# Kernel tuning notes

Hardware: AMD Instinct MI355X
Metric: run time of the kernel (lower is better)

Reference implementation:

```python
import jax, jax.numpy as jnp
import numpy as np

H = 256                      # latent_channels = LSTM hidden
OC = [32, 64, 64, 128]       # out_channels per mesh level
V = [5023, 1256, 314, 79, 20]  # vertex counts per level (fine -> coarse)
L = 9                        # spiral length
T = 64                       # audio frames (batch for decoder)


def setup_inputs() -> dict:
    key = jax.random.key(0)
    ks = iter(jax.random.split(key, 80))
    f32 = jnp.float32

    def nrm(shape, fan_in):
        return jax.random.normal(next(ks), shape, f32) * (1.0 / np.sqrt(fan_in))

    inp = {}
    inp['audio'] = jax.random.normal(next(ks), (T, 768), f32)
    inp['actor'] = jax.random.normal(next(ks), (V[0], 3), f32)

    # 5-layer bidirectional LSTM; layer 0 input 768, layers 1-4 input 2H
    inp['lstm_Wih0'] = nrm((2, 4 * H, 768), 768)
    inp['lstm_Whh0'] = nrm((2, 4 * H, H), H)
    inp['lstm_b0'] = jnp.zeros((2, 4 * H), f32)
    inp['lstm_Wih'] = nrm((4, 2, 4 * H, 2 * H), 2 * H)
    inp['lstm_Whh'] = nrm((4, 2, 4 * H, H), H)
    inp['lstm_b'] = jnp.zeros((4, 2, 4 * H), f32)

    # decoder entry fc: 2*latent -> num_vert * oc[-1]
    inp['fc_W'] = nrm((V[4] * OC[3], 2 * H), 2 * H)
    inp['fc_b'] = jnp.zeros((V[4] * OC[3],), f32)

    # SpiralConv weights (torch Linear layout: [out, in*L])
    inp['conv3_W'] = nrm((128, 128 * L), 128 * L); inp['conv3_b'] = jnp.zeros((128,), f32)
    inp['conv2_W'] = nrm((64, 128 * L), 128 * L);  inp['conv2_b'] = jnp.zeros((64,), f32)
    inp['conv1_W'] = nrm((64, 64 * L), 64 * L);    inp['conv1_b'] = jnp.zeros((64,), f32)
    inp['conv0_W'] = nrm((32, 64 * L), 64 * L);    inp['conv0_b'] = jnp.zeros((32,), f32)
    inp['head_W'] = nrm((3, 32 * L), 32 * L);      inp['head_b'] = jnp.zeros((3,), f32)

    # spiral indices per level: [V_j, L] with values in [0, V_j)
    for j in range(4):
        inp[f'idx{j}'] = jax.random.randint(next(ks), (V[j], L), 0, V[j], jnp.int32)

    # up_transform[j] sparse [V_j, V_{j+1}], ~3 nnz per row (COO)
    for j in range(4):
        nnz = 3 * V[j]
        inp[f'rows{j}'] = jnp.repeat(jnp.arange(V[j], dtype=jnp.int32), 3)
        inp[f'cols{j}'] = jax.random.randint(next(ks), (nnz,), 0, V[j + 1], jnp.int32)
        inp[f'vals{j}'] = jax.random.uniform(next(ks), (nnz,), f32) / 3.0
    return inp


def _lstm_dir(x, Wih, Whh, b, reverse):
    # x: [T, Din]; torch gate order i, f, g, o
    def step(carry, xt):
        h, c = carry
        g = Wih @ xt + Whh @ h + b            # [4H]
        i, f, gg, o = jnp.split(g, 4)
        c = jax.nn.sigmoid(f) * c + jax.nn.sigmoid(i) * jnp.tanh(gg)
        h = jax.nn.sigmoid(o) * jnp.tanh(c)
        return (h, c), h
    init = (jnp.zeros((H,), x.dtype), jnp.zeros((H,), x.dtype))
    _, hs = jax.lax.scan(step, init, x, reverse=reverse)
    return hs  # [T, H], aligned with input order


def _bilstm(x, Wih, Whh, b):
    hf = _lstm_dir(x, Wih[0], Whh[0], b[0], False)
    hb = _lstm_dir(x, Wih[1], Whh[1], b[1], True)
    return jnp.concatenate([hf, hb], axis=-1)  # [T, 2H]


def _pool(x, rows, cols, vals, n_out):
    # sparse up-transform: out[t, r] = sum_nnz vals * x[t, cols]
    g = x[:, cols, :] * vals[None, :, None]                       # [T, nnz, C]
    return jax.ops.segment_sum(g.swapaxes(0, 1), rows, num_segments=n_out).swapaxes(0, 1)


def _spiral(x, idx, W, b):
    # gather fixed spiral neighborhoods then dense linear
    g = x[:, idx, :].reshape(x.shape[0], idx.shape[0], -1)        # [T, V, L*C]
    return g @ W.T + b


def reference(audio, actor, lstm_Wih0, lstm_Whh0, lstm_b0, lstm_Wih, lstm_Whh, lstm_b,
              fc_W, fc_b, conv3_W, conv3_b, conv2_W, conv2_b, conv1_W, conv1_b,
              conv0_W, conv0_b, head_W, head_b,
              vals3, vals2, vals1, vals0,
              idx0, idx1, idx2, idx3,
              rows3, cols3, rows2, cols2, rows1, cols1, rows0, cols0):
    # audio embedding: 5-layer bidirectional LSTM (batch = 1)
    z = _bilstm(audio, lstm_Wih0, lstm_Whh0, lstm_b0)
    for l in range(4):
        z = _bilstm(z, lstm_Wih[l], lstm_Whh[l], lstm_b[l])       # [T, 2H]

    # decode
    x = (z @ fc_W.T + fc_b).reshape(z.shape[0], V[4], OC[3])      # [T, 20, 128]
    x = jax.nn.elu(_spiral(_pool(x, rows3, cols3, vals3, V[3]), idx3, conv3_W, conv3_b))
    x = jax.nn.elu(_spiral(_pool(x, rows2, cols2, vals2, V[2]), idx2, conv2_W, conv2_b))
    x = jax.nn.elu(_spiral(_pool(x, rows1, cols1, vals1, V[1]), idx1, conv1_W, conv1_b))
    x = jax.nn.elu(_spiral(_pool(x, rows0, cols0, vals0, V[0]), idx0, conv0_W, conv0_b))
    x = _spiral(x, idx0, head_W, head_b)                          # [T, 5023, 3]
    return x + actor[None]
```

## Files before the change

kernel.cpp:

```cpp
#include <hip/hip_runtime.h>
#include <hip/hip_bf16.h>

typedef __attribute__((ext_vector_type(8))) __bf16 bf16x8;
typedef __attribute__((ext_vector_type(4))) float  f32x4;
typedef __attribute__((ext_vector_type(4))) int    i32x4;

#define SCOPE_AGENT __HIP_MEMORY_SCOPE_AGENT

static __device__ __forceinline__ f32x4 mfma16(bf16x8 a, bf16x8 b, f32x4 c) {
    return __builtin_amdgcn_mfma_f32_16x16x32_bf16(a, b, c, 0, 0, 0);
}
static __device__ __forceinline__ i32x4 mfma_i8(i32x4 a, i32x4 b, i32x4 c) {
    return __builtin_amdgcn_mfma_i32_16x16x64_i8(a, b, c, 0, 0, 0);
}
static __device__ __forceinline__ float sigm(float x)  { return 1.0f / (1.0f + __expf(-x)); }
static __device__ __forceinline__ float tanh_(float x) { return 1.0f - 2.0f / (__expf(2.0f * x) + 1.0f); }

static __device__ __forceinline__ bf16x8 cvt8(const float* __restrict__ p) {
    const float4* q = (const float4*)p;
    float4 a = q[0], b = q[1];
    bf16x8 r;
    r[0] = (__bf16)a.x; r[1] = (__bf16)a.y; r[2] = (__bf16)a.z; r[3] = (__bf16)a.w;
    r[4] = (__bf16)b.x; r[5] = (__bf16)b.y; r[6] = (__bf16)b.z; r[7] = (__bf16)b.w;
    return r;
}
static __device__ __forceinline__ void signal_add(unsigned int* p) {
    __hip_atomic_fetch_add(p, 1u, __ATOMIC_RELEASE, SCOPE_AGENT);
}
template <int SLP>
static __device__ __forceinline__ void wait_eq(unsigned int* p, unsigned int v) {
    while (__hip_atomic_load(p, __ATOMIC_RELAXED, SCOPE_AGENT) != v)
        __builtin_amdgcn_s_sleep(SLP);
    (void)__hip_atomic_load(p, __ATOMIC_ACQUIRE, SCOPE_AGENT);
}
union g4u { unsigned long long q; __bf16 h[4]; };

#define ZBUF_OFF   1024
#define GX_OFF     132096
#define CONVW_OFF  66560
#define ARENA_A    621248
#define ARENA_B    21195456
#define WHHQ_BOFF  11534336
#define SWP_BOFF   14155776

__global__ __launch_bounds__(256) void precvt_whh(
    const float* __restrict__ Whh0, const float* __restrict__ WhhL,
    signed char* __restrict__ WhhQ, float* __restrict__ swp)
{
    const int g  = blockIdx.x * 4 + (threadIdx.x >> 6);
    const int dl = g >> 10;
    const int r  = g & 1023;
    const int lane = threadIdx.x & 63;
    const float* src = (dl < 2 ? Whh0 + (size_t)dl * 262144
                               : WhhL + (size_t)(dl - 2) * 262144) + (size_t)r * 256;
    float4 v = *(const float4*)(src + lane * 4);
    float am = fmaxf(fmaxf(fabsf(v.x), fabsf(v.y)), fmaxf(fabsf(v.z), fabsf(v.w)));
    #pragma unroll
    for (int m = 1; m < 64; m <<= 1) am = fmaxf(am, __shfl_xor(am, m));
    const float inv = am > 0.f ? 127.f / am : 0.f;
    int q0 = __float2int_rn(v.x * inv), q1 = __float2int_rn(v.y * inv);
    int q2 = __float2int_rn(v.z * inv), q3 = __float2int_rn(v.w * inv);
    unsigned pk = (q0 & 255) | ((q1 & 255) << 8) | ((q2 & 255) << 16) | ((q3 & 255) << 24);
    const int gate = r >> 8, cell = r & 255;
    const int m  = cell * 4 + gate;
    const int ln = m & 15, mt = m >> 4;
    const int k  = lane * 4;
    const int kc = k >> 6, quad = (k >> 4) & 3, j = k & 15;
    size_t addr = ((((size_t)dl * 64 + mt) * 4 + kc) * 64 + (quad * 16 + ln)) * 16 + j;
    *(unsigned*)(WhhQ + addr) = pk;
    if (lane == 0) swp[(size_t)dl * 1024 + cell * 4 + gate] = am / 127.f;
}

__global__ __launch_bounds__(256) void precvt_dec(
    const float* __restrict__ fcW, const float* __restrict__ c3W,
    const float* __restrict__ c2W, const float* __restrict__ c1W,
    const float* __restrict__ c0W, const float* __restrict__ hW,
    __bf16* __restrict__ fcWb, __bf16* __restrict__ convWb)
{
    int f = (blockIdx.x * 256 + threadIdx.x) * 4;
    if (f >= 1588064) return;
    const float* src; int off; __bf16* dst; int doff;
    if (f < 1310720) { src = fcW; off = f; dst = fcWb; doff = f; }
    else {
        int g = f - 1310720; dst = convWb; doff = g;
        if (g < 147456)      { src = c3W; off = g; }
        else if (g < 221184) { src = c2W; off = g - 147456; }
        else if (g < 258048) { src = c1W; off = g - 221184; }
        else if (g < 276480) { src = c0W; off = g - 258048; }
        else                 { src = hW;  off = g - 276480; }
    }
    float4 v = *(const float4*)(src + off);
    g4u u;
    u.h[0] = (__bf16)v.x; u.h[1] = (__bf16)v.y; u.h[2] = (__bf16)v.z; u.h[3] = (__bf16)v.w;
    *(unsigned long long*)(dst + doff) = u.q;
}

__global__ __launch_bounds__(512) __attribute__((amdgpu_waves_per_eu(2, 2)))
void lstm_fused(
    const float* __restrict__ audio,
    const float* __restrict__ Wih0,
    const float* __restrict__ WihL,
    const signed char* __restrict__ WhhQ,
    const float* __restrict__ swp,
    const float* __restrict__ b0, const float* __restrict__ bL,
    unsigned short* __restrict__ Gx_g,
    unsigned int* __restrict__ flags,
    unsigned short* __restrict__ zbuf)
{
    const int bid = blockIdx.x;
    const int tid = threadIdx.x;
    const int wave = tid >> 6, lane = tid & 63, ln = lane & 15, quad = lane >> 4;

    __shared__ __align__(16) signed char    hq[2][256];
    __shared__ __align__(16) signed char    zq[16384];
    __shared__ __align__(16) unsigned short gx_l[65536];

    if (bid < 16) {
        const int dir = bid >> 3, sub = bid & 7;
        const int gmt = sub * 8 + wave;
        const int m_a = gmt * 16 + ln;
        const int r_a = (m_a & 3) * 256 + (m_a >> 2);

        {
            const float* Wih_l = Wih0 + (size_t)dir * 786432;
            const float* b_l   = b0 + (size_t)dir * 1024;
            f32x4 acc[4];
            #pragma unroll
            for (int nt = 0; nt < 4; ++nt) acc[nt] = (f32x4){0.f, 0.f, 0.f, 0.f};
            for (int kc = 0; kc < 24; ++kc) {
                const int k0 = kc * 32 + quad * 8;
                bf16x8 afr = cvt8(Wih_l + (size_t)r_a * 768 + k0);
                #pragma unroll
                for (int nt = 0; nt < 4; ++nt) {
                    const int t = nt * 16 + ln;
                    bf16x8 bfr = cvt8(audio + (size_t)t * 768 + k0);
                    acc[nt] = mfma16(afr, bfr, acc[nt]);
                }
            }
            float bv[4];
            #pragma unroll
            for (int reg = 0; reg < 4; ++reg) {
                const int m_row = gmt * 16 + quad * 4 + reg;
                bv[reg] = b_l[(m_row & 3) * 256 + (m_row >> 2)];
            }
            #pragma unroll
            for (int nt = 0; nt < 4; ++nt)
                #pragma unroll
                for (int reg = 0; reg < 4; ++reg) {
                    const int m_row = gmt * 16 + quad * 4 + reg;
                    const int t = nt * 16 + ln;
                    __bf16 v = (__bf16)(acc[nt][reg] + bv[reg]);
                    Gx_g[(size_t)dir * 65536 + t * 1024 + m_row] =
                        __builtin_bit_cast(unsigned short, v);
                }
            __syncthreads();
            if (tid == 0) { __threadfence(); signal_add(&flags[0 * 2 + dir]); }
        }

        for (int l = 1; l < 5; ++l) {
            const float* Wih_l = WihL + (size_t)((l - 1) * 2 + dir) * 524288;
            const float* b_l   = bL + (size_t)((l - 1) * 2 + dir) * 1024;
            bf16x8 afr[16];
            #pragma unroll
            for (int kc = 0; kc < 16; ++kc)
                afr[kc] = cvt8(Wih_l + (size_t)r_a * 512 + kc * 32 + quad * 8);
            if (tid == 0) wait_eq<4>(&flags[32 + (l - 1)], 2u);
            __syncthreads();
            const __bf16* zp = (const __bf16*)(zbuf + (size_t)((l - 1) & 1) * 32768);

            f32x4 acc[4];
            #pragma unroll
            for (int nt = 0; nt < 4; ++nt) acc[nt] = (f32x4){0.f, 0.f, 0.f, 0.f};
            #pragma unroll 4
            for (int kc = 0; kc < 16; ++kc) {
                const int k0 = kc * 32 + quad * 8;
                #pragma unroll
                for (int nt = 0; nt < 4; ++nt) {
                    const int t = nt * 16 + ln;
                    bf16x8 bfr = *(const bf16x8*)(zp + (size_t)t * 512 + k0);
                    acc[nt] = mfma16(afr[kc], bfr, acc[nt]);
                }
            }
            float bv[4];
            #pragma unroll
            for (int reg = 0; reg < 4; ++reg) {
                const int m_row = gmt * 16 + quad * 4 + reg;
                bv[reg] = b_l[(m_row & 3) * 256 + (m_row >> 2)];
            }
            #pragma unroll
            for (int nt = 0; nt < 4; ++nt)
                #pragma unroll
                for (int reg = 0; reg < 4; ++reg) {
                    const int m_row = gmt * 16 + quad * 4 + reg;
                    const int t = nt * 16 + ln;
                    __bf16 v = (__bf16)(acc[nt][reg] + bv[reg]);
                    Gx_g[(size_t)dir * 65536 + t * 1024 + m_row] =
                        __builtin_bit_cast(unsigned short, v);
                }
            __syncthreads();
            if (tid == 0) { __threadfence(); signal_add(&flags[l * 2 + dir]); }
        }
    } else {
        const int dir = bid - 16;
        const unsigned short* Gx_d = Gx_g + (size_t)dir * 65536;
        const bool owner = (ln < 8);
        const int cell = wave * 32 + ln * 4 + quad;
        const int gcell = owner ? cell : 0;
        const i32x4 czero = (i32x4){0, 0, 0, 0};

        for (int l = 0; l < 5; ++l) {
            const int dl = l * 2 + dir;
            i32x4 wf[8][4];
            const i32x4* wb = (const i32x4*)(WhhQ + (size_t)dl * 262144);
            #pragma unroll
            for (int i = 0; i < 8; ++i)
                #pragma unroll
                for (int kc = 0; kc < 4; ++kc)
                    wf[i][kc] = wb[(size_t)(((wave * 8 + i) * 4 + kc)) * 64 + lane];
            float sc0 = 0.f, sc1 = 0.f, sc2 = 0.f, sc3 = 0.f;
            if (owner) {
                float4 s4 = *(const float4*)(swp + (size_t)dl * 1024 + cell * 4);
                const float f = 1.f / 127.f;
                sc0 = s4.x * f; sc1 = s4.y * f; sc2 = s4.z * f; sc3 = s4.w * f;
            }
            if (tid == 0) wait_eq<1>(&flags[l * 2 + dir], 8u);
            __syncthreads();
            {
                const float4* src = (const float4*)Gx_d;
                float4* dst = (float4*)gx_l;
                #pragma unroll
                for (int i = 0; i < 16; ++i) dst[i * 512 + tid] = src[i * 512 + tid];
            }
            if (tid < 64) ((unsigned int*)hq[0])[tid] = 0;
            float cst = 0.f;
            __syncthreads();

            for (int s = 0; s < 64; ++s) {
                const int t = dir ? (63 - s) : s;
                const int cur = s & 1, nxt = cur ^ 1;
                g4u gx;
                gx.q = *(const unsigned long long*)&gx_l[t * 1024 + gcell * 4];
                i32x4 acc[8];
                {
                    i32x4 b0v = *(const i32x4*)&hq[cur][quad * 16];
                    #pragma unroll
                    for (int i = 0; i < 8; ++i) acc[i] = mfma_i8(wf[i][0], b0v, czero);
                }
                #pragma unroll
                for (int kc = 1; kc < 4; ++kc) {
                    i32x4 b = *(const i32x4*)&hq[cur][kc * 64 + quad * 16];
                    #pragma unroll
                    for (int i = 0; i < 8; ++i) acc[i] = mfma_i8(wf[i][kc], b, acc[i]);
                }
                i32x4 a = acc[0];
                #pragma unroll
                for (int j = 1; j < 8; ++j) if (ln == j) a = acc[j];
                if (owner) {
                    float gi = (float)a[0] * sc0 + (float)gx.h[0];
                    float gf = (float)a[1] * sc1 + (float)gx.h[1];
                    float gg = (float)a[2] * sc2 + (float)gx.h[2];
                    float go = (float)a[3] * sc3 + (float)gx.h[3];
                    cst = sigm(gf) * cst + sigm(gi) * tanh_(gg);
                    float h = sigm(go) * tanh_(cst);
                    int q = __float2int_rn(h * 127.f);
                    hq[nxt][cell] = (signed char)q;
                    zq[t * 256 + cell] = (signed char)q;
                }
                __syncthreads();
            }
            unsigned short* zl = zbuf + (size_t)(l & 1) * 32768;
            #pragma unroll
            for (int i = 0; i < 8; ++i) {
                const int idx = i * 512 + tid;
                const int tt = idx >> 6, cb = (idx & 63) * 4;
                unsigned u = ((const unsigned*)zq)[idx];
                g4u o;
                #pragma unroll
                for (int j = 0; j < 4; ++j) {
                    int b = (int)(signed char)(u >> (8 * j));
                    o.h[j] = (__bf16)((float)b * (1.f / 127.f));
                }
                *(unsigned long long*)(zl + (size_t)tt * 512 + dir * 256 + cb) = o.q;
            }
            __syncthreads();
            if (tid == 0) { __threadfence(); signal_add(&flags[32 + l]); }
        }
    }
}

__global__ __launch_bounds__(256) void fc_kernel(
    const __bf16* __restrict__ zb, const __bf16* __restrict__ W,
    const float* __restrict__ bb, __bf16* __restrict__ out)
{
    const int tid = threadIdx.x;
    const int wave = tid >> 6, lane = tid & 63, ln = lane & 15, quad = lane >> 4;
    const int nbase = blockIdx.x * 64;
    f32x4 acc[4];
    #pragma unroll
    for (int nt = 0; nt < 4; nt++) acc[nt] = (f32x4){0.f, 0.f, 0.f, 0.f};
    #pragma unroll 2
    for (int kc = 0; kc < 16; kc++) {
        const int k0 = kc * 32 + quad * 8;
        bf16x8 a = *(const bf16x8*)(zb + (size_t)(wave * 16 + ln) * 512 + k0);
        #pragma unroll
        for (int nt = 0; nt < 4; nt++) {
            bf16x8 b = *(const bf16x8*)(W + (size_t)(nbase + nt * 16 + ln) * 512 + k0);
            acc[nt] = mfma16(a, b, acc[nt]);
        }
    }
    #pragma unroll
    for (int nt = 0; nt < 4; nt++) {
        const int n = nbase + nt * 16 + ln;
        const float bv = bb[n];
        #pragma unroll
        for (int reg = 0; reg < 4; reg++) {
            const int t = wave * 16 + quad * 4 + reg;
            out[(size_t)((n >> 7) * 64 + t) * 128 + (n & 127)] = (__bf16)(acc[nt][reg] + bv);
        }
    }
}

template <int C>
__global__ __launch_bounds__(256) void pool_kernel(
    const __bf16* __restrict__ in, __bf16* __restrict__ out,
    const int* __restrict__ cols, const float* __restrict__ vals, int V)
{
    const int P = 64 * C / 8;
    const int gid = blockIdx.x * 256 + threadIdx.x;
    if (gid >= V * P) return;
    const int r = gid / P;
    const int rem = gid - r * P;
    float acc[8] = {0.f, 0.f, 0.f, 0.f, 0.f, 0.f, 0.f, 0.f};
    #pragma unroll
    for (int s = 0; s < 3; s++) {
        const int col = cols[3 * r + s];
        const float vv = vals[3 * r + s];
        bf16x8 x = *(const bf16x8*)(in + (size_t)col * 64 * C + rem * 8);
        #pragma unroll
        for (int e = 0; e < 8; e++) acc[e] += vv * (float)x[e];
    }
    bf16x8 ov;
    #pragma unroll
    for (int e = 0; e < 8; e++) ov[e] = (__bf16)acc[e];
    *(bf16x8*)(out + (size_t)r * 64 * C + rem * 8) = ov;
}

template <int CIN, int COUT>
__global__ __launch_bounds__(256) void conv_kernel(
    const __bf16* __restrict__ in, __bf16* __restrict__ out,
    const int* __restrict__ idx, const __bf16* __restrict__ W,
    const float* __restrict__ bias)
{
    constexpr int K = 9 * CIN;
    constexpr int NT = COUT / 16;
    constexpr int NKC = K / 32;
    const int v = blockIdx.x;
    const int tid = threadIdx.x;
    const int wave = tid >> 6, lane = tid & 63, ln = lane & 15, quad = lane >> 4;
    __shared__ int sIdx[9];
    if (tid < 9) sIdx[tid] = idx[v * 9 + tid];
    __syncthreads();
    f32x4 acc[NT];
    #pragma unroll
    for (int nt = 0; nt < NT; nt++) acc[nt] = (f32x4){0.f, 0.f, 0.f, 0.f};
    const int tt = wave * 16 + ln;
    for (int kc = 0; kc < NKC; kc++) {
        const int k0 = kc * 32;
        const int l = k0 / CIN;
        const int c = (k0 & (CIN - 1)) + quad * 8;
        const int row = sIdx[l];
        bf16x8 a = *(const bf16x8*)(in + ((size_t)row * 64 + tt) * CIN + c);
        #pragma unroll
        for (int nt = 0; nt < NT; nt++) {
            bf16x8 b = *(const bf16x8*)(W + (size_t)(nt * 16 + ln) * K + k0 + quad * 8);
            acc[nt] = mfma16(a, b, acc[nt]);
        }
    }
    #pragma unroll
    for (int nt = 0; nt < NT; nt++) {
        const int n = nt * 16 + ln;
        const float bv = bias[n];
        #pragma unroll
        for (int reg = 0; reg < 4; reg++) {
            const int t = wave * 16 + quad * 4 + reg;
            float val = acc[nt][reg] + bv;
            val = val > 0.f ? val : (__expf(val) - 1.f);
            out[((size_t)v * 64 + t) * COUT + n] = (__bf16)val;
        }
    }
}

__global__ __launch_bounds__(256) void head_kernel(
    const __bf16* __restrict__ in, float* __restrict__ out,
    const int* __restrict__ idx, const __bf16* __restrict__ W,
    const float* __restrict__ bias, const float* __restrict__ actor)
{
    const int v = blockIdx.x;
    const int tid = threadIdx.x;
    const int wave = tid >> 6, lane = tid & 63, ln = lane & 15, quad = lane >> 4;
    __shared__ int sIdx[9];
    if (tid < 9) sIdx[tid] = idx[v * 9 + tid];
    __syncthreads();
    f32x4 acc = (f32x4){0.f, 0.f, 0.f, 0.f};
    const int tt = wave * 16 + ln;
    const int rown = ln < 3 ? ln : 0;
    #pragma unroll
    for (int kc = 0; kc < 9; kc++) {
        const int row = sIdx[kc];
        bf16x8 a = *(const bf16x8*)(in + ((size_t)row * 64 + tt) * 32 + quad * 8);
        bf16x8 b = *(const bf16x8*)(W + (size_t)rown * 288 + kc * 32 + quad * 8);
        acc = mfma16(a, b, acc);
    }
    if (ln < 3) {
        const float bv = bias[ln];
        const float av = actor[v * 3 + ln];
        #pragma unroll
        for (int reg = 0; reg < 4; reg++) {
            const int t = wave * 16 + quad * 4 + reg;
            out[((size_t)t * 5023 + v) * 3 + ln] = acc[reg] + bv + av;
        }
    }
}

extern "C" void kernel_launch(void* const* d_in, const int* in_sizes, int n_in,
                              void* d_out, int out_size, void* d_ws, size_t ws_size,
                              hipStream_t stream) {
    const float* audio = (const float*)d_in[0];
    const float* actor = (const float*)d_in[1];
    const float* Wih0  = (const float*)d_in[2];
    const float* Whh0  = (const float*)d_in[3];
    const float* b0    = (const float*)d_in[4];
    const float* WihL  = (const float*)d_in[5];
    const float* WhhL  = (const float*)d_in[6];
    const float* bLs   = (const float*)d_in[7];
    const float* fcW   = (const float*)d_in[8];
    const float* fcb   = (const float*)d_in[9];
    const float* c3W = (const float*)d_in[10]; const float* c3b = (const float*)d_in[11];
    const float* c2W = (const float*)d_in[12]; const float* c2b = (const float*)d_in[13];
    const float* c1W = (const float*)d_in[14]; const float* c1b = (const float*)d_in[15];
    const float* c0W = (const float*)d_in[16]; const float* c0b = (const float*)d_in[17];
    const float* hW  = (const float*)d_in[18]; const float* hb  = (const float*)d_in[19];
    const int* idx0 = (const int*)d_in[20];
    const int* idx1 = (const int*)d_in[21];
    const int* idx2 = (const int*)d_in[22];
    const int* idx3 = (const int*)d_in[23];
    const int* cols0 = (const int*)d_in[25]; const float* vals0 = (const float*)d_in[26];
    const int* cols1 = (const int*)d_in[28]; const float* vals1 = (const float*)d_in[29];
    const int* cols2 = (const int*)d_in[31]; const float* vals2 = (const float*)d_in[32];
    const int* cols3 = (const int*)d_in[34]; const float* vals3 = (const float*)d_in[35];

    char* ws = (char*)d_ws;
    unsigned int*   flags = (unsigned int*)ws;
    unsigned short* zbuf  = (unsigned short*)(ws + ZBUF_OFF);
    unsigned short* GxG   = (unsigned short*)(ws + GX_OFF);
    __bf16*         convWb = (__bf16*)(ws + CONVW_OFF);
    char* arenaA = ws + ARENA_A;
    char* arenaB = ws + ARENA_B;

    signed char* whhq = (signed char*)(arenaB + WHHQ_BOFF);
    float*       swp  = (float*)(arenaB + SWP_BOFF);
    __bf16*      fcWb = (__bf16*)(arenaB + 2097152);

    __bf16* x4b = (__bf16*)arenaA;
    __bf16* p3  = (__bf16*)arenaB;
    __bf16* c3o = (__bf16*)arenaA;
    __bf16* p2  = (__bf16*)arenaB;
    __bf16* c2o = (__bf16*)arenaA;
    __bf16* p1  = (__bf16*)arenaB;
    __bf16* c1o = (__bf16*)arenaA;
    __bf16* p0  = (__bf16*)arenaB;
    __bf16* c0o = (__bf16*)arenaA;

    (void)hipMemsetAsync(ws, 0, 1024, stream);

    precvt_whh<<<2560, 256, 0, stream>>>(Whh0, WhhL, whhq, swp);
    lstm_fused<<<18, 512, 0, stream>>>(audio, Wih0, WihL, whhq, swp, b0, bLs,
                                       GxG, flags, zbuf);
    precvt_dec<<<1552, 256, 0, stream>>>(fcW, c3W, c2W, c1W, c0W, hW, fcWb, convWb);

    fc_kernel<<<40, 256, 0, stream>>>((const __bf16*)zbuf, fcWb, fcb, x4b);

    { int n = 79 * 64 * 128 / 8;
      pool_kernel<128><<<(n + 255) / 256, 256, 0, stream>>>(x4b, p3, cols3, vals3, 79);
      conv_kernel<128, 128><<<79, 256, 0, stream>>>(p3, c3o, idx3, convWb + 0, c3b); }
    { int n = 314 * 64 * 128 / 8;
      pool_kernel<128><<<(n + 255) / 256, 256, 0, stream>>>(c3o, p2, cols2, vals2, 314);
      conv_kernel<128, 64><<<314, 256, 0, stream>>>(p2, c2o, idx2, convWb + 147456, c2b); }
    { int n = 1256 * 64 * 64 / 8;
      pool_kernel<64><<<(n + 255) / 256, 256, 0, stream>>>(c2o, p1, cols1, vals1, 1256);
      conv_kernel<64, 64><<<1256, 256, 0, stream>>>(p1, c1o, idx1, convWb + 221184, c1b); }
    { int n = 5023 * 64 * 64 / 8;
      pool_kernel<64><<<(n + 255) / 256, 256, 0, stream>>>(c1o, p0, cols0, vals0, 5023);
      conv_kernel<64, 32><<<5023, 256, 0, stream>>>(p0, c0o, idx0, convWb + 258048, c0b); }

    head_kernel<<<5023, 256, 0, stream>>>(c0o, (float*)d_out, idx0, convWb + 276480, hb, actor);
}
```

Before: 946.7 us.

## Replace int8 MFMA recurrent matvec with per-thread sdot4 dot products

The LSTM recurrent step previously ran a 16x16x64 int8 MFMA over eight tiles, and only 8 of 16 lanes used the results. It now gives each thread two gate rows of the quantized Whh, held in registers as 32 i32x4, and accumulates with sdot4 against the int8 hidden state broadcast from LDS. The quantized weight layout is changed to plain row-major to match. Gate activations are split across thread pairs and exchanged with a shuffle. This removes MFMA latency and wasted lanes on the serial critical path, at the cost of heavy register use and 64 scalar dot instructions per thread per step.

```diff
diff --git a/kernel.cpp b/kernel.cpp
--- a/kernel.cpp
+++ b/kernel.cpp
@@ -9,9 +9,6 @@
 
 static __device__ __forceinline__ f32x4 mfma16(bf16x8 a, bf16x8 b, f32x4 c) {
     return __builtin_amdgcn_mfma_f32_16x16x32_bf16(a, b, c, 0, 0, 0);
-}
-static __device__ __forceinline__ i32x4 mfma_i8(i32x4 a, i32x4 b, i32x4 c) {
-    return __builtin_amdgcn_mfma_i32_16x16x64_i8(a, b, c, 0, 0, 0);
 }
 static __device__ __forceinline__ float sigm(float x)  { return 1.0f / (1.0f + __expf(-x)); }
 static __device__ __forceinline__ float tanh_(float x) { return 1.0f - 2.0f / (__expf(2.0f * x) + 1.0f); }
@@ -63,12 +60,8 @@
     unsigned pk = (q0 & 255) | ((q1 & 255) << 8) | ((q2 & 255) << 16) | ((q3 & 255) << 24);
     const int gate = r >> 8, cell = r & 255;
     const int m  = cell * 4 + gate;
-    const int ln = m & 15, mt = m >> 4;
-    const int k  = lane * 4;
-    const int kc = k >> 6, quad = (k >> 4) & 3, j = k & 15;
-    size_t addr = ((((size_t)dl * 64 + mt) * 4 + kc) * 64 + (quad * 16 + ln)) * 16 + j;
-    *(unsigned*)(WhhQ + addr) = pk;
-    if (lane == 0) swp[(size_t)dl * 1024 + cell * 4 + gate] = am / 127.f;
+    *(unsigned*)(WhhQ + ((size_t)dl * 1024 + m) * 256 + lane * 4) = pk;
+    if (lane == 0) swp[(size_t)dl * 1024 + m] = am / 127.f;
 }
 
 __global__ __launch_bounds__(256) void precvt_dec(
@@ -203,26 +196,22 @@
     } else {
         const int dir = bid - 16;
         const unsigned short* Gx_d = Gx_g + (size_t)dir * 65536;
-        const bool owner = (ln < 8);
-        const int cell = wave * 32 + ln * 4 + quad;
-        const int gcell = owner ? cell : 0;
-        const i32x4 czero = (i32x4){0, 0, 0, 0};
+        const int c  = tid >> 1;
+        const int gp = tid & 1;
+        const int m0 = c * 4 + gp * 2;
 
         for (int l = 0; l < 5; ++l) {
             const int dl = l * 2 + dir;
-            i32x4 wf[8][4];
-            const i32x4* wb = (const i32x4*)(WhhQ + (size_t)dl * 262144);
-            #pragma unroll
-            for (int i = 0; i < 8; ++i)
-                #pragma unroll
-                for (int kc = 0; kc < 4; ++kc)
-                    wf[i][kc] = wb[(size_t)(((wave * 8 + i) * 4 + kc)) * 64 + lane];
-            float sc0 = 0.f, sc1 = 0.f, sc2 = 0.f, sc3 = 0.f;
-            if (owner) {
-                float4 s4 = *(const float4*)(swp + (size_t)dl * 1024 + cell * 4);
-                const float f = 1.f / 127.f;
-                sc0 = s4.x * f; sc1 = s4.y * f; sc2 = s4.z * f; sc3 = s4.w * f;
-            }
+            const i32x4* wb = (const i32x4*)(WhhQ + (size_t)dl * 262144 + (size_t)m0 * 256);
+            i32x4 w0[16], w1[16];
+            #pragma unroll
+            for (int q = 0; q < 16; ++q) w0[q] = wb[q];
+            #pragma unroll
+            for (int q = 0; q < 16; ++q) w1[q] = wb[16 + q];
+            float2 scp = *(const float2*)(swp + (size_t)dl * 1024 + m0);
+            const float s0 = scp.x * (1.f / 127.f);
+            const float s1 = scp.y * (1.f / 127.f);
+
             if (tid == 0) wait_eq<1>(&flags[l * 2 + dir], 8u);
             __syncthreads();
             {
@@ -238,33 +227,37 @@
             for (int s = 0; s < 64; ++s) {
                 const int t = dir ? (63 - s) : s;
                 const int cur = s & 1, nxt = cur ^ 1;
-                g4u gx;
-                gx.q = *(const unsigned long long*)&gx_l[t * 1024 + gcell * 4];
-                i32x4 acc[8];
-                {
-                    i32x4 b0v = *(const i32x4*)&hq[cur][quad * 16];
-                    #pragma unroll
-                    for (int i = 0; i < 8; ++i) acc[i] = mfma_i8(wf[i][0], b0v, czero);
-                }
-                #pragma unroll
-                for (int kc = 1; kc < 4; ++kc) {
-                    i32x4 b = *(const i32x4*)&hq[cur][kc * 64 + quad * 16];
-                    #pragma unroll
-                    for (int i = 0; i < 8; ++i) acc[i] = mfma_i8(wf[i][kc], b, acc[i]);
-                }
-                i32x4 a = acc[0];
-                #pragma unroll
-                for (int j = 1; j < 8; ++j) if (ln == j) a = acc[j];
-                if (owner) {
-                    float gi = (float)a[0] * sc0 + (float)gx.h[0];
-                    float gf = (float)a[1] * sc1 + (float)gx.h[1];
-                    float gg = (float)a[2] * sc2 + (float)gx.h[2];
-                    float go = (float)a[3] * sc3 + (float)gx.h[3];
-                    cst = sigm(gf) * cst + sigm(gi) * tanh_(gg);
-                    float h = sigm(go) * tanh_(cst);
-                    int q = __float2int_rn(h * 127.f);
-                    hq[nxt][cell] = (signed char)q;
-                    zq[t * 256 + cell] = (signed char)q;
+                const i32x4* hp = (const i32x4*)&hq[cur][0];
+                int acc0 = 0, acc1 = 0;
+                #pragma unroll
+                for (int q = 0; q < 16; ++q) {
+                    i32x4 hv = hp[q];
+                    acc0 = __builtin_amdgcn_sdot4(w0[q][0], hv[0], acc0, false);
+                    acc0 = __builtin_amdgcn_sdot4(w0[q][1], hv[1], acc0, false);
+                    acc0 = __builtin_amdgcn_sdot4(w0[q][2], hv[2], acc0, false);
+                    acc0 = __builtin_amdgcn_sdot4(w0[q][3], hv[3], acc0, false);
+                    acc1 = __builtin_amdgcn_sdot4(w1[q][0], hv[0], acc1, false);
+                    acc1 = __builtin_amdgcn_sdot4(w1[q][1], hv[1], acc1, false);
+                    acc1 = __builtin_amdgcn_sdot4(w1[q][2], hv[2], acc1, false);
+                    acc1 = __builtin_amdgcn_sdot4(w1[q][3], hv[3], acc1, false);
+                }
+                const unsigned gxp = *(const unsigned*)&gx_l[t * 1024 + m0];
+                const float gx0 = (float)__builtin_bit_cast(__bf16, (unsigned short)(gxp & 0xffffu));
+                const float gx1 = (float)__builtin_bit_cast(__bf16, (unsigned short)(gxp >> 16));
+                const float g0 = (float)acc0 * s0 + gx0;
+                const float g1 = (float)acc1 * s1 + gx1;
+                const float x0 = gp ? 2.f * g0 : g0;
+                const float sv = sigm(x0);
+                const float a0 = gp ? 2.f * sv - 1.f : sv;
+                const float a1 = sigm(g1);
+                const float p0 = __shfl_xor(a0, 1);
+                const float p1 = __shfl_xor(a1, 1);
+                if (gp == 0) {
+                    cst = a1 * cst + a0 * p0;
+                    const float h = p1 * tanh_(cst);
+                    const int qv = __float2int_rn(h * 127.f);
+                    hq[nxt][c] = (signed char)qv;
+                    zq[t * 256 + c] = (signed char)qv;
                 }
                 __syncthreads();
             }
```

Measured after the change: 1.003 ms. 1.06x slower.

## Pipeline LSTM input projection per 16-timestep chunk with finer-grained flags

Applied to the files above, without the earlier changes.

The producer blocks now compute the input-gate projection in four 16-timestep chunks, ordered by scan direction, and raise a per-chunk flag after each. The recurrent block waits only for the chunk it needs before copying it into a smaller shared buffer, so the sequential scan can start before the whole projection is done. Hidden outputs are now written straight to global bf16 instead of being staged in shared memory and converted at the end. The layer-0 projection also preloads the weight fragments and uses two accumulators. In exchange there are more flag waits and barriers inside the serial loop, and scattered 2-byte global stores on every step.

```diff
diff --git a/kernel.cpp b/kernel.cpp
--- a/kernel.cpp
+++ b/kernel.cpp
@@ -112,49 +112,50 @@
     const int wave = tid >> 6, lane = tid & 63, ln = lane & 15, quad = lane >> 4;
 
     __shared__ __align__(16) signed char    hq[2][256];
-    __shared__ __align__(16) signed char    zq[16384];
-    __shared__ __align__(16) unsigned short gx_l[65536];
+    __shared__ __align__(16) unsigned short gx_l[16384];
 
     if (bid < 16) {
         const int dir = bid >> 3, sub = bid & 7;
         const int gmt = sub * 8 + wave;
         const int m_a = gmt * 16 + ln;
         const int r_a = (m_a & 3) * 256 + (m_a >> 2);
+        unsigned short* GxO = Gx_g + (size_t)dir * 65536;
 
         {
             const float* Wih_l = Wih0 + (size_t)dir * 786432;
             const float* b_l   = b0 + (size_t)dir * 1024;
-            f32x4 acc[4];
+            bf16x8 afr[24];
             #pragma unroll
-            for (int nt = 0; nt < 4; ++nt) acc[nt] = (f32x4){0.f, 0.f, 0.f, 0.f};
-            for (int kc = 0; kc < 24; ++kc) {
-                const int k0 = kc * 32 + quad * 8;
-                bf16x8 afr = cvt8(Wih_l + (size_t)r_a * 768 + k0);
-                #pragma unroll
-                for (int nt = 0; nt < 4; ++nt) {
-                    const int t = nt * 16 + ln;
-                    bf16x8 bfr = cvt8(audio + (size_t)t * 768 + k0);
-                    acc[nt] = mfma16(afr, bfr, acc[nt]);
-                }
-            }
+            for (int kc = 0; kc < 24; ++kc)
+                afr[kc] = cvt8(Wih_l + (size_t)r_a * 768 + kc * 32 + quad * 8);
             float bv[4];
             #pragma unroll
             for (int reg = 0; reg < 4; ++reg) {
                 const int m_row = gmt * 16 + quad * 4 + reg;
                 bv[reg] = b_l[(m_row & 3) * 256 + (m_row >> 2)];
             }
-            #pragma unroll
-            for (int nt = 0; nt < 4; ++nt)
+            for (int ii = 0; ii < 4; ++ii) {
+                const int nt = dir ? 3 - ii : ii;
+                const int t  = nt * 16 + ln;
+                f32x4 acA = (f32x4){0.f, 0.f, 0.f, 0.f};
+                f32x4 acB = (f32x4){0.f, 0.f, 0.f, 0.f};
+                #pragma unroll
+                for (int kc = 0; kc < 24; kc += 2) {
+                    acA = mfma16(afr[kc],
+                                 cvt8(audio + (size_t)t * 768 + kc * 32 + quad * 8), acA);
+                    acB = mfma16(afr[kc + 1],
+                                 cvt8(audio + (size_t)t * 768 + (kc + 1) * 32 + quad * 8), acB);
+                }
+                f32x4 acc = acA + acB;
                 #pragma unroll
                 for (int reg = 0; reg < 4; ++reg) {
                     const int m_row = gmt * 16 + quad * 4 + reg;
-                    const int t = nt * 16 + ln;
-                    __bf16 v = (__bf16)(acc[nt][reg] + bv[reg]);
-                    Gx_g[(size_t)dir * 65536 + t * 1024 + m_row] =
-                        __builtin_bit_cast(unsigned short, v);
-                }
-            __syncthreads();
-            if (tid == 0) { __threadfence(); signal_add(&flags[0 * 2 + dir]); }
+                    __bf16 v = (__bf16)(acc[reg] + bv[reg]);
+                    GxO[(size_t)t * 1024 + m_row] = __builtin_bit_cast(unsigned short, v);
+                }
+                __syncthreads();
+                if (tid == 0) { __threadfence(); signal_add(&flags[(0 * 2 + dir) * 4 + nt]); }
+            }
         }
 
         for (int l = 1; l < 5; ++l) {
@@ -164,41 +165,38 @@
             #pragma unroll
             for (int kc = 0; kc < 16; ++kc)
                 afr[kc] = cvt8(Wih_l + (size_t)r_a * 512 + kc * 32 + quad * 8);
-            if (tid == 0) wait_eq<4>(&flags[32 + (l - 1)], 2u);
-            __syncthreads();
-            const __bf16* zp = (const __bf16*)(zbuf + (size_t)((l - 1) & 1) * 32768);
-
-            f32x4 acc[4];
-            #pragma unroll
-            for (int nt = 0; nt < 4; ++nt) acc[nt] = (f32x4){0.f, 0.f, 0.f, 0.f};
-            #pragma unroll 4
-            for (int kc = 0; kc < 16; ++kc) {
-                const int k0 = kc * 32 + quad * 8;
-                #pragma unroll
-                for (int nt = 0; nt < 4; ++nt) {
-                    const int t = nt * 16 + ln;
-                    bf16x8 bfr = *(const bf16x8*)(zp + (size_t)t * 512 + k0);
-                    acc[nt] = mfma16(afr[kc], bfr, acc[nt]);
-                }
-            }
             float bv[4];
             #pragma unroll
             for (int reg = 0; reg < 4; ++reg) {
                 const int m_row = gmt * 16 + quad * 4 + reg;
                 bv[reg] = b_l[(m_row & 3) * 256 + (m_row >> 2)];
             }
-            #pragma unroll
-            for (int nt = 0; nt < 4; ++nt)
+            if (tid == 0) wait_eq<4>(&flags[48 + (l - 1)], 2u);
+            __syncthreads();
+            const __bf16* zp = (const __bf16*)(zbuf + (size_t)((l - 1) & 1) * 32768);
+
+            for (int ii = 0; ii < 4; ++ii) {
+                const int nt = dir ? 3 - ii : ii;
+                const int t  = nt * 16 + ln;
+                f32x4 acA = (f32x4){0.f, 0.f, 0.f, 0.f};
+                f32x4 acB = (f32x4){0.f, 0.f, 0.f, 0.f};
+                #pragma unroll
+                for (int kc = 0; kc < 16; kc += 2) {
+                    acA = mfma16(afr[kc],
+                                 *(const bf16x8*)(zp + (size_t)t * 512 + kc * 32 + quad * 8), acA);
+                    acB = mfma16(afr[kc + 1],
+                                 *(const bf16x8*)(zp + (size_t)t * 512 + (kc + 1) * 32 + quad * 8), acB);
+                }
+                f32x4 acc = acA + acB;
                 #pragma unroll
                 for (int reg = 0; reg < 4; ++reg) {
                     const int m_row = gmt * 16 + quad * 4 + reg;
-                    const int t = nt * 16 + ln;
-                    __bf16 v = (__bf16)(acc[nt][reg] + bv[reg]);
-                    Gx_g[(size_t)dir * 65536 + t * 1024 + m_row] =
-                        __builtin_bit_cast(unsigned short, v);
-                }
-            __syncthreads();
-            if (tid == 0) { __threadfence(); signal_add(&flags[l * 2 + dir]); }
+                    __bf16 v = (__bf16)(acc[reg] + bv[reg]);
+                    GxO[(size_t)t * 1024 + m_row] = __builtin_bit_cast(unsigned short, v);
+                }
+                __syncthreads();
+                if (tid == 0) { __threadfence(); signal_add(&flags[(l * 2 + dir) * 4 + nt]); }
+            }
         }
     } else {
         const int dir = bid - 16;
@@ -223,23 +221,27 @@
                 const float f = 1.f / 127.f;
                 sc0 = s4.x * f; sc1 = s4.y * f; sc2 = s4.z * f; sc3 = s4.w * f;
             }
-            if (tid == 0) wait_eq<1>(&flags[l * 2 + dir], 8u);
-            __syncthreads();
-            {
-                const float4* src = (const float4*)Gx_d;
-                float4* dst = (float4*)gx_l;
-                #pragma unroll
-                for (int i = 0; i < 16; ++i) dst[i * 512 + tid] = src[i * 512 + tid];
-            }
             if (tid < 64) ((unsigned int*)hq[0])[tid] = 0;
             float cst = 0.f;
-            __syncthreads();
+            unsigned short* zl = zbuf + (size_t)(l & 1) * 32768;
+            const int gxbase = (l * 2 + dir) * 4;
 
             for (int s = 0; s < 64; ++s) {
+                if ((s & 15) == 0) {
+                    const int nt = dir ? 3 - (s >> 4) : (s >> 4);
+                    if (tid == 0) wait_eq<1>(&flags[gxbase + nt], 8u);
+                    __syncthreads();
+                    const float4* src = (const float4*)(Gx_d + (size_t)nt * 16384);
+                    float4* dst = (float4*)gx_l;
+                    #pragma unroll
+                    for (int i = 0; i < 4; ++i) dst[i * 512 + tid] = src[i * 512 + tid];
+                    __syncthreads();
+                }
                 const int t = dir ? (63 - s) : s;
+                const int tl = t & 15;
                 const int cur = s & 1, nxt = cur ^ 1;
                 g4u gx;
-                gx.q = *(const unsigned long long*)&gx_l[t * 1024 + gcell * 4];
+                gx.q = *(const unsigned long long*)&gx_l[tl * 1024 + gcell * 4];
                 i32x4 acc[8];
                 {
                     i32x4 b0v = *(const i32x4*)&hq[cur][quad * 16];
@@ -264,26 +266,13 @@
                     float h = sigm(go) * tanh_(cst);
                     int q = __float2int_rn(h * 127.f);
                     hq[nxt][cell] = (signed char)q;
-                    zq[t * 256 + cell] = (signed char)q;
+                    __bf16 zv = (__bf16)((float)q * (1.f / 127.f));
+                    zl[(size_t)t * 512 + dir * 256 + cell] =
+                        __builtin_bit_cast(unsigned short, zv);
                 }
                 __syncthreads();
             }
-            unsigned short* zl = zbuf + (size_t)(l & 1) * 32768;
-            #pragma unroll
-            for (int i = 0; i < 8; ++i) {
-                const int idx = i * 512 + tid;
-                const int tt = idx >> 6, cb = (idx & 63) * 4;
-                unsigned u = ((const unsigned*)zq)[idx];
-                g4u o;
-                #pragma unroll
-                for (int j = 0; j < 4; ++j) {
-                    int b = (int)(signed char)(u >> (8 * j));
-                    o.h[j] = (__bf16)((float)b * (1.f / 127.f));
-                }
-                *(unsigned long long*)(zl + (size_t)tt * 512 + dir * 256 + cb) = o.q;
-            }
-            __syncthreads();
-            if (tid == 0) { __threadfence(); signal_add(&flags[32 + l]); }
+            if (tid == 0) { __threadfence(); signal_add(&flags[48 + l]); }
         }
     }
 }
```

Measured after the change: 851.9 us. 10.0% less time.
